# Kernel optimization log

Measured on AMD Instinct MI355X. Metric: run time of the kernel, lower is better.

Reference implementation:

```python
import jax, jax.numpy as jnp
import numpy as np

DIM, HEADS, DHEAD, CTX_DIM, DFF = 1280, 20, 64, 768, 5120
EPS = 1e-5
SCALE = DHEAD ** -0.5


def layer_norm(x, g, b):
    mu = jnp.mean(x, axis=-1, keepdims=True)
    var = jnp.mean(jnp.square(x - mu), axis=-1, keepdims=True)
    return (x - mu) * jax.lax.rsqrt(var + EPS) * g + b


def cross_attention(x, ctx, wq, wk, wv, wo, bo):
    B, N, _ = x.shape
    M = ctx.shape[1]
    q = jnp.einsum('bne,ef->bnf', x, wq).reshape(B, N, HEADS, DHEAD).transpose(0, 2, 1, 3)
    k = jnp.einsum('bme,ef->bmf', ctx, wk).reshape(B, M, HEADS, DHEAD).transpose(0, 2, 1, 3)
    v = jnp.einsum('bme,ef->bmf', ctx, wv).reshape(B, M, HEADS, DHEAD).transpose(0, 2, 1, 3)
    scores = jnp.einsum('bhnd,bhmd->bhnm', q, k) * SCALE
    attn = jax.nn.softmax(scores, axis=-1)
    out = jnp.einsum('bhnm,bhmd->bhnd', attn, v)
    out = out.transpose(0, 2, 1, 3).reshape(B, N, HEADS * DHEAD)
    return jnp.einsum('bnf,fe->bne', out, wo) + bo


def geglu_ff(x, w1, b1, w2, b2):
    h = jnp.einsum('bne,ef->bnf', x, w1) + b1  # [B,N,2*DFF]
    a, gate = h[..., :DFF], h[..., DFF:]
    h = a * jax.nn.gelu(gate)
    return jnp.einsum('bnf,fe->bne', h, w2) + b2


def block_forward(x, context,
                  g1, be1, wq1, wk1, wv1, wo1, bo1,
                  g2, be2, wq2, wk2, wv2, wo2, bo2,
                  g3, be3, w_ff1, b_ff1, w_ff2, b_ff2):
    x = cross_attention(layer_norm(x, g1, be1), layer_norm(x, g1, be1), wq1, wk1, wv1, wo1, bo1) + x
    x = cross_attention(layer_norm(x, g2, be2), context, wq2, wk2, wv2, wo2, bo2) + x
    return geglu_ff(layer_norm(x, g3, be3), w_ff1, b_ff1, w_ff2, b_ff2) + x


def setup_inputs() -> dict:
    key = jax.random.key(0)
    ks = jax.random.split(key, 20)
    s = 0.02
    inner = HEADS * DHEAD
    return {
        'x': jax.random.normal(ks[0], (4, 1024, DIM), jnp.float32),
        'context': jax.random.normal(ks[1], (4, 77, CTX_DIM), jnp.float32),
        'g1': jnp.ones((DIM,), jnp.float32), 'be1': jnp.zeros((DIM,), jnp.float32),
        'wq1': jax.random.normal(ks[2], (DIM, inner), jnp.float32) * s,
        'wk1': jax.random.normal(ks[3], (DIM, inner), jnp.float32) * s,
        'wv1': jax.random.normal(ks[4], (DIM, inner), jnp.float32) * s,
        'wo1': jax.random.normal(ks[5], (inner, DIM), jnp.float32) * s,
        'bo1': jnp.zeros((DIM,), jnp.float32),
        'g2': jnp.ones((DIM,), jnp.float32), 'be2': jnp.zeros((DIM,), jnp.float32),
        'wq2': jax.random.normal(ks[6], (DIM, inner), jnp.float32) * s,
        'wk2': jax.random.normal(ks[7], (CTX_DIM, inner), jnp.float32) * s,
        'wv2': jax.random.normal(ks[8], (CTX_DIM, inner), jnp.float32) * s,
        'wo2': jax.random.normal(ks[9], (inner, DIM), jnp.float32) * s,
        'bo2': jnp.zeros((DIM,), jnp.float32),
        'g3': jnp.ones((DIM,), jnp.float32), 'be3': jnp.zeros((DIM,), jnp.float32),
        'w_ff1': jax.random.normal(ks[10], (DIM, 2 * DFF), jnp.float32) * s,
        'b_ff1': jnp.zeros((2 * DFF,), jnp.float32),
        'w_ff2': jax.random.normal(ks[11], (DFF, DIM), jnp.float32) * s,
        'b_ff2': jnp.zeros((DIM,), jnp.float32),
    }


def reference(x, context,
              g1, be1, wq1, wk1, wv1, wo1, bo1,
              g2, be2, wq2, wk2, wv2, wo2, bo2,
              g3, be3, w_ff1, b_ff1, w_ff2, b_ff2):
    return block_forward(x, context,
                         g1, be1, wq1, wk1, wv1, wo1, bo1,
                         g2, be2, wq2, wk2, wv2, wo2, bo2,
                         g3, be3, w_ff1, b_ff1, w_ff2, b_ff2)
```

## Files before the change

### kernel.cpp

```cpp
#include <hip/hip_runtime.h>

typedef unsigned short u16;
typedef __bf16 bf16x8 __attribute__((ext_vector_type(8)));
typedef float f32x4 __attribute__((ext_vector_type(4)));

static __device__ __forceinline__ float bf2f(u16 u) {
    union { unsigned int i; float f; } v; v.i = ((unsigned int)u) << 16; return v.f;
}
static __device__ __forceinline__ u16 f2bf(float f) {
    union { float f; unsigned int i; } v; v.f = f;
    unsigned int b = v.i;
    b += 0x7fffu + ((b >> 16) & 1u);
    return (u16)(b >> 16);
}
static __device__ __forceinline__ u16 ldbf(const void* p, size_t i, int isf32) {
    return isf32 ? f2bf(((const float*)p)[i]) : ((const u16*)p)[i];
}
static __device__ __forceinline__ float ldf(const void* p, size_t i, int isf32) {
    return isf32 ? ((const float*)p)[i] : bf2f(((const u16*)p)[i]);
}
static __device__ __forceinline__ void glds16(const u16* g, u16* l) {
    __builtin_amdgcn_global_load_lds(
        (const __attribute__((address_space(1))) unsigned int*)g,
        (__attribute__((address_space(3))) unsigned int*)l,
        16, 0, 0);
}
static __device__ __forceinline__ int xcd_swz(int lid, int nwg) {
    return ((nwg & 7) == 0) ? ((lid & 7) * (nwg >> 3) + (lid >> 3)) : lid;
}

__global__ __launch_bounds__(256) void k_detect(const u16* __restrict__ xu, int* __restrict__ flag) {
    u16 v = xu[threadIdx.x * 2];
    int e = (v >> 7) & 0xFF;
    int sane = (e >= 87 && e <= 133) ? 1 : 0;
    int total = __syncthreads_count(sane);
    if (threadIdx.x == 0) flag[0] = (total < 192) ? 1 : 0;
}

__global__ __launch_bounds__(256) void k_b2f(const void* __restrict__ in, float* __restrict__ out, int n,
                                             const int* __restrict__ flagp) {
    int isf32 = *flagp;
    int i = blockIdx.x * 256 + threadIdx.x;
    if (i < n) out[i] = ldf(in, i, isf32);
}

__global__ __launch_bounds__(256) void k_cvt(const void* __restrict__ in, u16* __restrict__ out, int n,
                                             const int* __restrict__ flagp) {
    int isf32 = *flagp;
    int i = blockIdx.x * 256 + threadIdx.x;
    if (i < n) out[i] = ldbf(in, i, isf32);
}

__global__ __launch_bounds__(256) void k_addp(float* __restrict__ X, const float* __restrict__ P, int n4) {
    int i = blockIdx.x * 256 + threadIdx.x;
    int stride = gridDim.x * 256;
    for (; i < n4; i += stride) {
        f32x4 a = ((const f32x4*)X)[i];
        f32x4 b = ((const f32x4*)P)[i];
        a[0] += b[0]; a[1] += b[1]; a[2] += b[2]; a[3] += b[3];
        ((f32x4*)X)[i] = a;
    }
}

__global__ __launch_bounds__(256) void k_transpose(const void* __restrict__ W, u16* __restrict__ Wt,
                                                   int K, int N, const int* __restrict__ flagp) {
    int isf32 = *flagp;
    __shared__ u16 T[32][33];
    int k0 = blockIdx.x * 32, n0 = blockIdx.y * 32;
    int tid = threadIdx.x;
    int c = tid & 31, rr = tid >> 5;
    #pragma unroll
    for (int j = 0; j < 4; ++j) {
        int k = rr + j * 8;
        T[k][c] = ldbf(W, (size_t)(k0 + k) * N + n0 + c, isf32);
    }
    __syncthreads();
    #pragma unroll
    for (int j = 0; j < 4; ++j) {
        int n = rr + j * 8;
        Wt[(size_t)(n0 + n) * K + k0 + c] = T[c][n];
    }
}

__global__ __launch_bounds__(256) void k_transpose3(const void* __restrict__ W0, const void* __restrict__ W1,
                                                    const void* __restrict__ W2,
                                                    u16* __restrict__ D0, u16* __restrict__ D1,
                                                    u16* __restrict__ D2,
                                                    int K, int N, const int* __restrict__ flagp) {
    int isf32 = *flagp;
    int z = blockIdx.z;
    const void* W = (z == 0) ? W0 : (z == 1) ? W1 : W2;
    u16* Wt = (z == 0) ? D0 : (z == 1) ? D1 : D2;
    __shared__ u16 T[32][33];
    int k0 = blockIdx.x * 32, n0 = blockIdx.y * 32;
    int tid = threadIdx.x;
    int c = tid & 31, rr = tid >> 5;
    #pragma unroll
    for (int j = 0; j < 4; ++j) {
        int k = rr + j * 8;
        T[k][c] = ldbf(W, (size_t)(k0 + k) * N + n0 + c, isf32);
    }
    __syncthreads();
    #pragma unroll
    for (int j = 0; j < 4; ++j) {
        int n = rr + j * 8;
        Wt[(size_t)(n0 + n) * K + k0 + c] = T[c][n];
    }
}

__global__ __launch_bounds__(256) void k_layernorm(float* __restrict__ X, const float* __restrict__ P,
                                                   const void* __restrict__ G, const void* __restrict__ Bb,
                                                   u16* __restrict__ Y, int D,
                                                   const int* __restrict__ flagp) {
    int isf32 = *flagp;
    int row = blockIdx.x;
    float* xr = X + (size_t)row * D;
    const float* pr = P ? (P + (size_t)row * D) : nullptr;
    float s = 0.f, s2 = 0.f;
    for (int i = threadIdx.x; i < D; i += 256) {
        float v = xr[i] + (P ? pr[i] : 0.f);
        s += v; s2 += v * v;
    }
    #pragma unroll
    for (int off = 32; off; off >>= 1) { s += __shfl_down(s, off); s2 += __shfl_down(s2, off); }
    __shared__ float rs[4], rs2[4];
    __shared__ float stat[2];
    int w = threadIdx.x >> 6;
    if ((threadIdx.x & 63) == 0) { rs[w] = s; rs2[w] = s2; }
    __syncthreads();
    if (threadIdx.x == 0) {
        float ts = rs[0] + rs[1] + rs[2] + rs[3];
        float ts2 = rs2[0] + rs2[1] + rs2[2] + rs2[3];
        float mu = ts / D;
        float var = ts2 / D - mu * mu;
        stat[0] = mu; stat[1] = rsqrtf(var + 1e-5f);
    }
    __syncthreads();
    float mu = stat[0], rstd = stat[1];
    u16* yr = Y + (size_t)row * D;
    for (int i = threadIdx.x; i < D; i += 256) {
        float v = xr[i] + (P ? pr[i] : 0.f);
        if (P) xr[i] = v;
        yr[i] = f2bf((v - mu) * rstd * ldf(G, i, isf32) + ldf(Bb, i, isf32));
    }
}

template <int EPI>
__global__ __launch_bounds__(512, 2) void k_gemm8(const u16* __restrict__ A, const u16* __restrict__ Bt,
                                                  void* __restrict__ Cout, const void* __restrict__ bias,
                                                  int M, int N, int K, const int* __restrict__ flagp) {
    __shared__ __align__(16) u16 sm[65536];
    const int tid = threadIdx.x;
    const int w = tid >> 6;
    const int lane = tid & 63;
    const int quad = lane >> 4, r = lane & 15;
    const int wm = w >> 2, wn = w & 3;
    const int lid = blockIdx.x + blockIdx.y * gridDim.x;
    const int nid = xcd_swz(lid, gridDim.x * gridDim.y);
    const int row0 = (nid % gridDim.x) * 256;
    const int col0 = (nid / gridDim.x) * 256;
    const int NT = K >> 6;

    const u16* aP[2][2];
    const u16* bP[2][2];
    #pragma unroll
    for (int j = 0; j < 2; ++j) {
        int c = tid + w * 64 + j * 64;
        int rj = c >> 3;
        int qe = (c & 7) ^ (rj & 7);
        #pragma unroll
        for (int h = 0; h < 2; ++h) {
            int gr = h * 128 + rj;
            aP[h][j] = A + (size_t)(row0 + gr) * K + qe * 8;
            int n = col0 + gr;
            int m = (EPI == 1) ? (((n >> 4) & 1) * 5120 + (n >> 5) * 16 + (n & 15)) : n;
            bP[h][j] = Bt + (size_t)m * K + qe * 8;
        }
    }
    auto stageA = [&](int h, int t) {
        u16* base = sm + (t & 1) * 32768 + h * 8192 + w * 1024;
        glds16(aP[h][0] + t * 64, base);
        glds16(aP[h][1] + t * 64, base + 512);
    };
    auto stageB = [&](int h, int t) {
        u16* base = sm + (t & 1) * 32768 + 16384 + h * 8192 + w * 1024;
        glds16(bP[h][0] + t * 64, base);
        glds16(bP[h][1] + t * 64, base + 512);
    };

    f32x4 acc[2][2][4][2] = {};
    const int xq = r & 7;
    bf16x8 afA[4][2], afB[4][2], bf0[2][2], bf1[2][2];

    auto readA = [&](bf16x8 (&dst)[4][2], int Ab, int half) {
        #pragma unroll
        for (int i = 0; i < 4; ++i) {
            int ar = half * 128 + wm * 64 + i * 16 + r;
            #pragma unroll
            for (int ks = 0; ks < 2; ++ks)
                dst[i][ks] = *(const bf16x8*)(sm + Ab + ar * 64 + (((ks * 4 + quad) ^ xq) * 8));
        }
    };
    auto readB = [&](bf16x8 (&dst)[2][2], int Bb, int half) {
        #pragma unroll
        for (int g = 0; g < 2; ++g) {
            int br = half * 128 + wn * 32 + g * 16 + r;
            #pragma unroll
            for (int ks = 0; ks < 2; ++ks)
                dst[g][ks] = *(const bf16x8*)(sm + Bb + br * 64 + (((ks * 4 + quad) ^ xq) * 8));
        }
    };
    auto domfma = [&](int qm, int qn, bf16x8 (&a)[4][2], bf16x8 (&b)[2][2]) {
        #pragma unroll
        for (int ks = 0; ks < 2; ++ks)
            #pragma unroll
            for (int i = 0; i < 4; ++i)
                #pragma unroll
                for (int g = 0; g < 2; ++g)
                    acc[qm][qn][i][g] = __builtin_amdgcn_mfma_f32_16x16x32_bf16(
                        a[i][ks], b[g][ks], acc[qm][qn][i][g], 0, 0, 0);
    };

    stageA(0, 0); stageB(0, 0); stageA(1, 0); stageB(1, 0);
    if (NT > 1) {
        stageA(0, 1); stageB(0, 1);
        asm volatile("s_waitcnt vmcnt(4)" ::: "memory");
    } else {
        asm volatile("s_waitcnt vmcnt(0)" ::: "memory");
    }
    __builtin_amdgcn_s_barrier();
    readA(afA, 0, 0);
    readB(bf0, 16384, 0);

    for (int t = 0; t < NT; ++t) {
        const int Ab = (t & 1) * 32768;
        const int Bb = Ab + 16384;
        const int Abn = ((t + 1) & 1) * 32768;
        readB(bf1, Bb, 1);
        __builtin_amdgcn_sched_barrier(0);
        __builtin_amdgcn_s_setprio(1);
        domfma(0, 0, afA, bf0);
        __builtin_amdgcn_s_setprio(0);
        if (t + 1 < NT) stageA(1, t + 1);
        __builtin_amdgcn_s_barrier();
        readA(afB, Ab, 1);
        __builtin_amdgcn_sched_barrier(0);
        __builtin_amdgcn_s_setprio(1);
        domfma(0, 1, afA, bf1);
        __builtin_amdgcn_s_setprio(0);
        if (t + 1 < NT) stageB(1, t + 1);
        __builtin_amdgcn_s_barrier();
        __builtin_amdgcn_s_setprio(1);
        domfma(1, 1, afB, bf1);
        __builtin_amdgcn_s_setprio(0);
        if (t + 2 < NT) stageA(0, t + 2);
        __builtin_amdgcn_s_barrier();
        __builtin_amdgcn_s_setprio(1);
        domfma(1, 0, afB, bf0);
        __builtin_amdgcn_s_setprio(0);
        if (t + 2 < NT) stageB(0, t + 2);
        if (t + 2 < NT) asm volatile("s_waitcnt vmcnt(4)" ::: "memory");
        else            asm volatile("s_waitcnt vmcnt(0)" ::: "memory");
        __builtin_amdgcn_s_barrier();
        if (t + 1 < NT) {
            readA(afA, Abn, 0);
            readB(bf0, Abn + 16384, 0);
        }
    }

    if (EPI == 0) {
        u16* C = (u16*)Cout;
        #pragma unroll
        for (int qm = 0; qm < 2; ++qm) {
            #pragma unroll
            for (int qn = 0; qn < 2; ++qn) {
                #pragma unroll
                for (int i = 0; i < 4; ++i) {
                    int grow = row0 + qm * 128 + wm * 64 + i * 16 + quad * 4;
                    #pragma unroll
                    for (int g = 0; g < 2; ++g) {
                        int gcol = col0 + qn * 128 + wn * 32 + g * 16 + r;
                        #pragma unroll
                        for (int t4 = 0; t4 < 4; ++t4)
                            C[(size_t)(grow + t4) * N + gcol] = f2bf(acc[qm][qn][i][g][t4]);
                    }
                }
            }
        }
    } else {
        const int isf32 = *flagp;
        u16* C = (u16*)Cout;
        #pragma unroll
        for (int qm = 0; qm < 2; ++qm) {
            #pragma unroll
            for (int qn = 0; qn < 2; ++qn) {
                int ncb = col0 + qn * 128 + wn * 32;
                int oc = (ncb >> 1) + r;
                float bva = ldf(bias, oc, isf32);
                float bvu = ldf(bias, 5120 + oc, isf32);
                #pragma unroll
                for (int i = 0; i < 4; ++i) {
                    int grow = row0 + qm * 128 + wm * 64 + i * 16 + quad * 4;
                    #pragma unroll
                    for (int t4 = 0; t4 < 4; ++t4) {
                        float a = acc[qm][qn][i][0][t4] + bva;
                        float u = acc[qm][qn][i][1][t4] + bvu;
                        float z2 = 1.5957691216f * (u + 0.044715f * u * u * u);
                        float gl = u * __builtin_amdgcn_rcpf(1.f + __expf(-z2));
                        C[(size_t)(grow + t4) * 5120 + oc] = f2bf(a * gl);
                    }
                }
            }
        }
    }
}

template <int EPI>
__global__ __launch_bounds__(256) void k_gemm_t(const u16* __restrict__ A, const u16* __restrict__ Bt,
                                                void* __restrict__ Cout, float* __restrict__ Rf,
                                                const void* __restrict__ bias,
                                                int M, int N, int K, const int* __restrict__ flagp) {
    int isf32 = *flagp;
    __shared__ __align__(16) u16 As[4096];
    __shared__ __align__(16) u16 Bs[4096];
    int tid = threadIdx.x;
    int row0 = blockIdx.x * 128, col0 = blockIdx.y * 128;
    int S = gridDim.z, kz = blockIdx.z;
    int kseg = K / S;
    int kb = kz * kseg, ke = kb + kseg;
    int wave = tid >> 6, lane = tid & 63;
    int wm = (wave >> 1) * 64, wn = (wave & 1) * 64;
    int quad = lane >> 4, r = lane & 15;
    int c0 = wave * 64 + lane, c1 = 256 + c0;
    int ar0 = c0 >> 2, aq0 = (c0 & 3) ^ ((ar0 >> 1) & 3);
    int ar1 = c1 >> 2, aq1 = (c1 & 3) ^ ((ar1 >> 1) & 3);
    const u16* Ag0 = A + (size_t)min(row0 + ar0, M - 1) * K + aq0 * 8;
    const u16* Ag1 = A + (size_t)min(row0 + ar1, M - 1) * K + aq1 * 8;
    const u16* Bg0 = Bt + (size_t)(col0 + ar0) * K + aq0 * 8;
    const u16* Bg1 = Bt + (size_t)(col0 + ar1) * K + aq1 * 8;
    u16* lA0 = As + wave * 512;
    u16* lA1 = As + 2048 + wave * 512;
    u16* lB0 = Bs + wave * 512;
    u16* lB1 = Bs + 2048 + wave * 512;
    f32x4 acc[4][4] = {};
    for (int k0 = kb; k0 < ke; k0 += 32) {
        __syncthreads();
        glds16(Ag0 + k0, lA0);
        glds16(Ag1 + k0, lA1);
        glds16(Bg0 + k0, lB0);
        glds16(Bg1 + k0, lB1);
        __syncthreads();
        bf16x8 af[4], bfv[4];
        #pragma unroll
        for (int i = 0; i < 4; ++i) {
            int row = wm + i * 16 + r;
            af[i] = *(const bf16x8*)(As + (row * 4 + (quad ^ ((row >> 1) & 3))) * 8);
        }
        #pragma unroll
        for (int g = 0; g < 4; ++g) {
            int row = wn + g * 16 + r;
            bfv[g] = *(const bf16x8*)(Bs + (row * 4 + (quad ^ ((row >> 1) & 3))) * 8);
        }
        #pragma unroll
        for (int i = 0; i < 4; ++i)
            #pragma unroll
            for (int g = 0; g < 4; ++g)
                acc[i][g] = __builtin_amdgcn_mfma_f32_16x16x32_bf16(af[i], bfv[g], acc[i][g], 0, 0, 0);
    }
    #pragma unroll
    for (int i = 0; i < 4; ++i) {
        int grow = row0 + wm + i * 16 + quad * 4;
        if (grow >= M) continue;
        #pragma unroll
        for (int g = 0; g < 4; ++g) {
            int gcol = col0 + wn + g * 16 + r;
            float bv = (EPI == 2 && kz == 0) ? ldf(bias, gcol, isf32) : 0.f;
            #pragma unroll
            for (int t = 0; t < 4; ++t) {
                float v = acc[i][g][t];
                size_t off = (size_t)(grow + t) * N + gcol;
                if (EPI == 0) {
                    ((u16*)Cout)[off] = f2bf(v);
                } else {
                    if (kz == 0) Rf[off] += v + bv;
                    else         ((float*)Cout)[off] = v;
                }
            }
        }
    }
}

__global__ __launch_bounds__(256) void k_geglu_t(const u16* __restrict__ A, const u16* __restrict__ Bt,
                                                 const void* __restrict__ bias, u16* __restrict__ Out,
                                                 int M, int K, const int* __restrict__ flagp) {
    const int Nout = 5120;
    int isf32 = *flagp;
    __shared__ __align__(16) u16 As[4096];
    __shared__ __align__(16) u16 Bs[4096];
    int tid = threadIdx.x;
    int row0 = blockIdx.x * 128, col0 = blockIdx.y * 64;
    int wave = tid >> 6, lane = tid & 63;
    int quad = lane >> 4, r = lane & 15;
    int c0 = wave * 64 + lane, c1 = 256 + c0;
    int ar0 = c0 >> 2, aq0 = (c0 & 3) ^ ((ar0 >> 1) & 3);
    int ar1 = c1 >> 2, aq1 = (c1 & 3) ^ ((ar1 >> 1) & 3);
    const u16* Ag0 = A + (size_t)min(row0 + ar0, M - 1) * K + aq0 * 8;
    const u16* Ag1 = A + (size_t)min(row0 + ar1, M - 1) * K + aq1 * 8;
    const u16* Bg0 = Bt + (size_t)((ar0 >> 6) * Nout + col0 + (ar0 & 63)) * K + aq0 * 8;
    const u16* Bg1 = Bt + (size_t)((ar1 >> 6) * Nout + col0 + (ar1 & 63)) * K + aq1 * 8;
    u16* lA0 = As + wave * 512;
    u16* lA1 = As + 2048 + wave * 512;
    u16* lB0 = Bs + wave * 512;
    u16* lB1 = Bs + 2048 + wave * 512;
    f32x4 acc[2][2][4] = {};
    for (int k0 = 0; k0 < K; k0 += 32) {
        __syncthreads();
        glds16(Ag0 + k0, lA0);
        glds16(Ag1 + k0, lA1);
        glds16(Bg0 + k0, lB0);
        glds16(Bg1 + k0, lB1);
        __syncthreads();
        bf16x8 af[2], bv[2][4];
        #pragma unroll
        for (int i = 0; i < 2; ++i) {
            int row = wave * 32 + i * 16 + r;
            af[i] = *(const bf16x8*)(As + (row * 4 + (quad ^ ((row >> 1) & 3))) * 8);
        }
        #pragma unroll
        for (int p = 0; p < 2; ++p)
            #pragma unroll
            for (int g = 0; g < 4; ++g) {
                int row = p * 64 + g * 16 + r;
                bv[p][g] = *(const bf16x8*)(Bs + (row * 4 + (quad ^ ((row >> 1) & 3))) * 8);
            }
        #pragma unroll
        for (int p = 0; p < 2; ++p)
            #pragma unroll
            for (int i = 0; i < 2; ++i)
                #pragma unroll
                for (int g = 0; g < 4; ++g)
                    acc[p][i][g] = __builtin_amdgcn_mfma_f32_16x16x32_bf16(af[i], bv[p][g], acc[p][i][g], 0, 0, 0);
    }
    #pragma unroll
    for (int i = 0; i < 2; ++i) {
        int grow = row0 + wave * 32 + i * 16 + quad * 4;
        #pragma unroll
        for (int g = 0; g < 4; ++g) {
            int gcol = col0 + g * 16 + r;
            float bva = ldf(bias, gcol, isf32);
            float bvu = ldf(bias, Nout + gcol, isf32);
            #pragma unroll
            for (int t = 0; t < 4; ++t) {
                float a = acc[0][i][g][t] + bva;
                float u = acc[1][i][g][t] + bvu;
                float z2 = 1.5957691216f * (u + 0.044715f * u * u * u);
                float gl = u * __builtin_amdgcn_rcpf(1.f + __expf(-z2));
                Out[(size_t)(grow + t) * Nout + gcol] = f2bf(a * gl);
            }
        }
    }
}

template <int EPI, bool AEXT>
__global__ __launch_bounds__(256) void k_gemm(const void* __restrict__ A, const void* __restrict__ B,
                                              void* __restrict__ Cout, float* __restrict__ Rf,
                                              const void* __restrict__ bias,
                                              int M, int N, int K, const int* __restrict__ flagp) {
    int isf32 = *flagp;
    __shared__ u16 As[64][40];
    __shared__ u16 Bs[64][40];
    int tid = threadIdx.x;
    int row0 = blockIdx.x * 64, col0 = blockIdx.y * 64;
    int wave = tid >> 6, lane = tid & 63;
    int wm = (wave >> 1) * 32, wn = (wave & 1) * 32;
    int quad = lane >> 4, r = lane & 15;
    int arow = tid >> 2, akk = (tid & 3) * 8;
    int bnl = tid & 63, bkk = (tid >> 6) * 8;
    int garow = row0 + arow;
    f32x4 acc[2][2] = {};
    for (int k0 = 0; k0 < K; k0 += 32) {
        uint4 aval = {0u, 0u, 0u, 0u};
        if (garow < M) {
            if (AEXT && isf32) {
                const float* Af = (const float*)A;
                u16 t[8];
                #pragma unroll
                for (int j = 0; j < 8; ++j) t[j] = f2bf(Af[(size_t)garow * K + k0 + akk + j]);
                aval = *(uint4*)t;
            } else {
                aval = *(const uint4*)((const u16*)A + (size_t)garow * K + k0 + akk);
            }
        }
        u16 btmp[8];
        #pragma unroll
        for (int j = 0; j < 8; ++j) btmp[j] = ldbf(B, (size_t)(k0 + bkk + j) * N + col0 + bnl, isf32);
        __syncthreads();
        *(uint4*)(&As[arow][akk]) = aval;
        *(uint4*)(&Bs[bnl][bkk]) = *(uint4*)btmp;
        __syncthreads();
        bf16x8 a0 = *(const bf16x8*)(&As[wm + r][quad * 8]);
        bf16x8 a1 = *(const bf16x8*)(&As[wm + 16 + r][quad * 8]);
        bf16x8 b0 = *(const bf16x8*)(&Bs[wn + r][quad * 8]);
        bf16x8 b1 = *(const bf16x8*)(&Bs[wn + 16 + r][quad * 8]);
        acc[0][0] = __builtin_amdgcn_mfma_f32_16x16x32_bf16(a0, b0, acc[0][0], 0, 0, 0);
        acc[0][1] = __builtin_amdgcn_mfma_f32_16x16x32_bf16(a0, b1, acc[0][1], 0, 0, 0);
        acc[1][0] = __builtin_amdgcn_mfma_f32_16x16x32_bf16(a1, b0, acc[1][0], 0, 0, 0);
        acc[1][1] = __builtin_amdgcn_mfma_f32_16x16x32_bf16(a1, b1, acc[1][1], 0, 0, 0);
    }
    #pragma unroll
    for (int i = 0; i < 2; ++i)
        #pragma unroll
        for (int jn = 0; jn < 2; ++jn)
            #pragma unroll
            for (int t = 0; t < 4; ++t) {
                int grow = row0 + wm + i * 16 + quad * 4 + t;
                int gcol = col0 + wn + jn * 16 + r;
                if (grow >= M) continue;
                float v = acc[i][jn][t];
                size_t off = (size_t)grow * N + gcol;
                if (EPI == 0) {
                    ((u16*)Cout)[off] = f2bf(v);
                } else if (EPI == 2) {
                    Rf[off] += v + ldf(bias, gcol, isf32);
                } else {
                    ((float*)Cout)[off] = v + ldf(bias, gcol, isf32) + Rf[off];
                }
            }
}

__global__ __launch_bounds__(256) void k_gemm_geglu(const u16* __restrict__ A, const void* __restrict__ B,
                                                    const void* __restrict__ bias, u16* __restrict__ Out,
                                                    int M, int Nout, int K, int ldb,
                                                    const int* __restrict__ flagp) {
    int isf32 = *flagp;
    __shared__ u16 As[64][40];
    __shared__ u16 Bs[64][40];
    int tid = threadIdx.x;
    int row0 = blockIdx.x * 64, col0 = blockIdx.y * 64;
    int wave = tid >> 6, lane = tid & 63;
    int wm = (wave >> 1) * 32, wn = (wave & 1) * 32;
    int quad = lane >> 4, r = lane & 15;
    int arow = tid >> 2, akk = (tid & 3) * 8;
    int bnl = tid & 63, bkk = (tid >> 6) * 8;
    int garow = row0 + arow;
    f32x4 acc[2][2][2] = {};
    for (int p = 0; p < 2; ++p) {
        for (int k0 = 0; k0 < K; k0 += 32) {
            uint4 aval = {0u, 0u, 0u, 0u};
            if (garow < M) aval = *(const uint4*)(A + (size_t)garow * K + k0 + akk);
            u16 btmp[8];
            #pragma unroll
            for (int j = 0; j < 8; ++j)
                btmp[j] = ldbf(B, (size_t)(k0 + bkk + j) * ldb + p * Nout + col0 + bnl, isf32);
            __syncthreads();
            *(uint4*)(&As[arow][akk]) = aval;
            *(uint4*)(&Bs[bnl][bkk]) = *(uint4*)btmp;
            __syncthreads();
            bf16x8 a0 = *(const bf16x8*)(&As[wm + r][quad * 8]);
            bf16x8 a1 = *(const bf16x8*)(&As[wm + 16 + r][quad * 8]);
            bf16x8 b0 = *(const bf16x8*)(&Bs[wn + r][quad * 8]);
            bf16x8 b1 = *(const bf16x8*)(&Bs[wn + 16 + r][quad * 8]);
            acc[p][0][0] = __builtin_amdgcn_mfma_f32_16x16x32_bf16(a0, b0, acc[p][0][0], 0, 0, 0);
            acc[p][0][1] = __builtin_amdgcn_mfma_f32_16x16x32_bf16(a0, b1, acc[p][0][1], 0, 0, 0);
            acc[p][1][0] = __builtin_amdgcn_mfma_f32_16x16x32_bf16(a1, b0, acc[p][1][0], 0, 0, 0);
            acc[p][1][1] = __builtin_amdgcn_mfma_f32_16x16x32_bf16(a1, b1, acc[p][1][1], 0, 0, 0);
        }
    }
    #pragma unroll
    for (int i = 0; i < 2; ++i)
        #pragma unroll
        for (int jn = 0; jn < 2; ++jn)
            #pragma unroll
            for (int t = 0; t < 4; ++t) {
                int grow = row0 + wm + i * 16 + quad * 4 + t;
                int gcol = col0 + wn + jn * 16 + r;
                if (grow >= M) continue;
                float a = acc[0][i][jn][t] + ldf(bias, gcol, isf32);
                float u = acc[1][i][jn][t] + ldf(bias, Nout + gcol, isf32);
                float th = tanhf(0.7978845608f * (u + 0.044715f * u * u * u));
                float gl = 0.5f * u * (1.f + th);
                Out[(size_t)grow * Nout + gcol] = f2bf(a * gl);
            }
}

__global__ __launch_bounds__(256) void k_attn_flash(const u16* __restrict__ Q, const u16* __restrict__ K,
                                                    const u16* __restrict__ V, u16* __restrict__ O,
                                                    int N, int Mkv, int H, int ldq, int ldkv, int ldo) {
    __shared__ u16 Sp[4][16][40];
    __shared__ u16 VT[64][40];
    int nt = N / 64;
    int qt = blockIdx.x % nt;
    int bh = blockIdx.x / nt;
    int h = bh % H, b = bh / H;
    int tid = threadIdx.x, wave = tid >> 6, lane = tid & 63;
    int quad = lane >> 4, r = lane & 15;
    int q0 = qt * 64 + wave * 16;

    const u16* qbase = Q + ((size_t)(b * N + q0 + r)) * ldq + h * 64;
    bf16x8 aq0 = *(const bf16x8*)(qbase + quad * 8);
    bf16x8 aq1 = *(const bf16x8*)(qbase + 32 + quad * 8);

    f32x4 accO[4] = {};
    float m_i[4] = {-1e30f, -1e30f, -1e30f, -1e30f};
    float l_i[4] = {0.f, 0.f, 0.f, 0.f};

    int vkv = tid & 31, vdg = tid >> 5;

    for (int kv0 = 0; kv0 < Mkv; kv0 += 32) {
        int kr0 = min(kv0 + r, Mkv - 1);
        int kr1 = min(kv0 + 16 + r, Mkv - 1);
        const u16* kb0 = K + ((size_t)(b * Mkv + kr0)) * ldkv + h * 64;
        const u16* kb1 = K + ((size_t)(b * Mkv + kr1)) * ldkv + h * 64;
        bf16x8 bk00 = *(const bf16x8*)(kb0 + quad * 8);
        bf16x8 bk01 = *(const bf16x8*)(kb0 + 32 + quad * 8);
        bf16x8 bk10 = *(const bf16x8*)(kb1 + quad * 8);
        bf16x8 bk11 = *(const bf16x8*)(kb1 + 32 + quad * 8);
        int vrow = min(kv0 + vkv, Mkv - 1);
        uint4 vv = *(const uint4*)(V + ((size_t)(b * Mkv + vrow)) * ldkv + h * 64 + vdg * 8);

        __syncthreads();
        VT[vdg * 8 + 0][vkv] = (u16)(vv.x);
        VT[vdg * 8 + 1][vkv] = (u16)(vv.x >> 16);
        VT[vdg * 8 + 2][vkv] = (u16)(vv.y);
        VT[vdg * 8 + 3][vkv] = (u16)(vv.y >> 16);
        VT[vdg * 8 + 4][vkv] = (u16)(vv.z);
        VT[vdg * 8 + 5][vkv] = (u16)(vv.z >> 16);
        VT[vdg * 8 + 6][vkv] = (u16)(vv.w);
        VT[vdg * 8 + 7][vkv] = (u16)(vv.w >> 16);
        __syncthreads();

        f32x4 s0 = {}, s1 = {};
        s0 = __builtin_amdgcn_mfma_f32_16x16x32_bf16(aq0, bk00, s0, 0, 0, 0);
        s0 = __builtin_amdgcn_mfma_f32_16x16x32_bf16(aq1, bk01, s0, 0, 0, 0);
        s1 = __builtin_amdgcn_mfma_f32_16x16x32_bf16(aq0, bk10, s1, 0, 0, 0);
        s1 = __builtin_amdgcn_mfma_f32_16x16x32_bf16(aq1, bk11, s1, 0, 0, 0);
        bool mask0 = (kv0 + r) >= Mkv;
        bool mask1 = (kv0 + 16 + r) >= Mkv;

        #pragma unroll
        for (int t = 0; t < 4; ++t) {
            float a = mask0 ? -1e30f : s0[t] * 0.125f;
            float c = mask1 ? -1e30f : s1[t] * 0.125f;
            float mx = fmaxf(a, c);
            mx = fmaxf(mx, __shfl_xor(mx, 1));
            mx = fmaxf(mx, __shfl_xor(mx, 2));
            mx = fmaxf(mx, __shfl_xor(mx, 4));
            mx = fmaxf(mx, __shfl_xor(mx, 8));
            float mn = fmaxf(m_i[t], mx);
            float alpha = __expf(m_i[t] - mn);
            float p0 = __expf(a - mn);
            float p1 = __expf(c - mn);
            float ps = p0 + p1;
            ps += __shfl_xor(ps, 1);
            ps += __shfl_xor(ps, 2);
            ps += __shfl_xor(ps, 4);
            ps += __shfl_xor(ps, 8);
            l_i[t] = l_i[t] * alpha + ps;
            m_i[t] = mn;
            accO[0][t] *= alpha; accO[1][t] *= alpha; accO[2][t] *= alpha; accO[3][t] *= alpha;
            Sp[wave][quad * 4 + t][r] = f2bf(p0);
            Sp[wave][quad * 4 + t][16 + r] = f2bf(p1);
        }

        bf16x8 ap = *(const bf16x8*)(&Sp[wave][r][quad * 8]);
        #pragma unroll
        for (int g = 0; g < 4; ++g) {
            bf16x8 bvv = *(const bf16x8*)(&VT[g * 16 + r][quad * 8]);
            accO[g] = __builtin_amdgcn_mfma_f32_16x16x32_bf16(ap, bvv, accO[g], 0, 0, 0);
        }
    }

    u16* ob = O + ((size_t)(b * N + q0)) * ldo + h * 64;
    #pragma unroll
    for (int t = 0; t < 4; ++t) {
        float inv = 1.f / l_i[t];
        #pragma unroll
        for (int g = 0; g < 4; ++g)
            ob[(size_t)(quad * 4 + t) * ldo + g * 16 + r] = f2bf(accO[g][t] * inv);
    }
}

extern "C" void kernel_launch(void* const* d_in, const int* in_sizes, int n_in,
                              void* d_out, int out_size, void* d_ws, size_t ws_size,
                              hipStream_t stream) {
    const void* x    = d_in[0];
    const void* ctx  = d_in[1];
    const void* g1   = d_in[2];
    const void* be1  = d_in[3];
    const void* wq1  = d_in[4];
    const void* wk1  = d_in[5];
    const void* wv1  = d_in[6];
    const void* wo1  = d_in[7];
    const void* bo1  = d_in[8];
    const void* g2   = d_in[9];
    const void* be2  = d_in[10];
    const void* wq2  = d_in[11];
    const void* wk2  = d_in[12];
    const void* wv2  = d_in[13];
    const void* wo2  = d_in[14];
    const void* bo2  = d_in[15];
    const void* g3   = d_in[16];
    const void* be3  = d_in[17];
    const void* wff1 = d_in[18];
    const void* bff1 = d_in[19];
    const void* wff2 = d_in[20];
    const void* bff2 = d_in[21];

    const int BT = 4096, D = 1280;
    dim3 blk(256);
    char* ws = (char*)d_ws;

    const size_t NEED_FAST = 117393664;
    if (ws_size >= NEED_FAST) {
        int*   flag   = (int*)(ws);
        u16* lnout    = (u16*)(ws + 256);
        u16* qkv      = (u16*)(ws + 10486016);
        u16* attnout  = (u16*)(ws + 10486016 + 31457280);
        u16* gbuf     = (u16*)(ws + 10486016);
        u16* ctxb     = (u16*)(ws + 52429056);
        u16* kv2      = (u16*)(ws + 52902144);
        u16* wqkv1t   = (u16*)(ws + 54479104);
        u16* wo1t     = (u16*)(ws + 64309504);
        u16* wq2t     = (u16*)(ws + 67586304);
        u16* wkv2t    = (u16*)(ws + 70863104);
        u16* wo2t     = (u16*)(ws + 74795264);
        u16* wff1t    = (u16*)(ws + 78072064);
        u16* wff2t    = (u16*)(ws + 104286464);
        float* pff2   = (float*)(ws + 54479104);
        float* pWO    = (float*)(ws + 10486016);
        float* xres   = (float*)d_out;

        k_detect<<<dim3(1), blk, 0, stream>>>((const u16*)x, flag);
        k_b2f<<<dim3((BT * D + 255) / 256), blk, 0, stream>>>(x, xres, BT * D, flag);
        k_transpose3<<<dim3(40, 40, 3), blk, 0, stream>>>(wq1, wk1, wv1,
                                                          wqkv1t, wqkv1t + 1280 * 1280,
                                                          wqkv1t + 2 * 1280 * 1280, 1280, 1280, flag);
        k_transpose3<<<dim3(40, 40, 3), blk, 0, stream>>>(wo1, wq2, wo2,
                                                          wo1t, wq2t, wo2t, 1280, 1280, flag);
        k_transpose3<<<dim3(24, 40, 2), blk, 0, stream>>>(wk2, wv2, wv2,
                                                          wkv2t, wkv2t + 1280 * 768,
                                                          wkv2t + 1280 * 768, 768, 1280, flag);
        k_transpose<<<dim3(40, 320), blk, 0, stream>>>(wff1, wff1t, 1280, 10240, flag);
        k_transpose<<<dim3(160, 40), blk, 0, stream>>>(wff2, wff2t, 5120, 1280, flag);
        k_cvt<<<dim3((308 * 768 + 255) / 256), blk, 0, stream>>>(ctx, ctxb, 308 * 768, flag);
        k_layernorm<<<dim3(BT), blk, 0, stream>>>(xres, nullptr, g1, be1, lnout, D, flag);
        k_gemm8<0><<<dim3(16, 15), dim3(512), 0, stream>>>(lnout, wqkv1t, qkv, nullptr, BT, 3840, D, flag);
        k_attn_flash<<<dim3(16 * 80), blk, 0, stream>>>(qkv, qkv + 1280, qkv + 2560, attnout,
                                                        1024, 1024, 20, 3840, 3840, 1280);
        k_gemm_t<2><<<dim3(32, 10, 2), blk, 0, stream>>>(attnout, wo1t, pWO, xres, bo1, BT, D, D, flag);
        k_layernorm<<<dim3(BT), blk, 0, stream>>>(xres, pWO, g2, be2, lnout, D, flag);
        k_gemm_t<0><<<dim3(32, 10), blk, 0, stream>>>(lnout, wq2t, qkv, nullptr, nullptr, BT, D, D, flag);
        k_gemm_t<0><<<dim3(3, 20), blk, 0, stream>>>(ctxb, wkv2t, kv2, nullptr, nullptr, 308, 2560, 768, flag);
        k_attn_flash<<<dim3(16 * 80), blk, 0, stream>>>(qkv, kv2, kv2 + 1280, attnout,
                                                        1024, 77, 20, 1280, 2560, 1280);
        k_gemm_t<2><<<dim3(32, 10, 2), blk, 0, stream>>>(attnout, wo2t, pWO, xres, bo2, BT, D, D, flag);
        k_layernorm<<<dim3(BT), blk, 0, stream>>>(xres, pWO, g3, be3, lnout, D, flag);
        k_gemm8<1><<<dim3(16, 40), dim3(512), 0, stream>>>(lnout, wff1t, gbuf, bff1, BT, 10240, D, flag);
        k_gemm_t<2><<<dim3(32, 10, 2), blk, 0, stream>>>(gbuf, wff2t, pff2, xres, bff2, BT, D, 5120, flag);
        k_addp<<<dim3(2048), blk, 0, stream>>>(xres, pff2, BT * D / 4);
    } else {
        int*   flag    = (int*)(ws);
        float* xres    = (float*)(ws + 256);
        u16* lnout     = (u16*)(ws + 20971776);
        u16* q         = (u16*)(ws + 31457536);
        u16* kbuf      = (u16*)(ws + 41943296);
        u16* vbuf      = (u16*)(ws + 52429056);
        u16* attnout   = (u16*)(ws + 62914816);
        u16* k2        = (u16*)(ws + 73400576);
        u16* v2        = (u16*)(ws + 74189056);
        u16* gbuf      = (u16*)(ws + 31457536);

        dim3 g_gemm(64, 20);
        dim3 g_kv(5, 20);
        dim3 g_attn(16 * 80);

        k_detect<<<dim3(1), blk, 0, stream>>>((const u16*)x, flag);
        k_b2f<<<dim3((BT * D + 255) / 256), blk, 0, stream>>>(x, xres, BT * D, flag);
        k_layernorm<<<dim3(BT), blk, 0, stream>>>(xres, nullptr, g1, be1, lnout, D, flag);
        k_gemm<0, false><<<g_gemm, blk, 0, stream>>>(lnout, wq1, q, nullptr, nullptr, BT, D, D, flag);
        k_gemm<0, false><<<g_gemm, blk, 0, stream>>>(lnout, wk1, kbuf, nullptr, nullptr, BT, D, D, flag);
        k_gemm<0, false><<<g_gemm, blk, 0, stream>>>(lnout, wv1, vbuf, nullptr, nullptr, BT, D, D, flag);
        k_attn_flash<<<g_attn, blk, 0, stream>>>(q, kbuf, vbuf, attnout, 1024, 1024, 20, 1280, 1280, 1280);
        k_gemm<2, false><<<g_gemm, blk, 0, stream>>>(attnout, wo1, nullptr, xres, bo1, BT, D, D, flag);
        k_layernorm<<<dim3(BT), blk, 0, stream>>>(xres, nullptr, g2, be2, lnout, D, flag);
        k_gemm<0, false><<<g_gemm, blk, 0, stream>>>(lnout, wq2, q, nullptr, nullptr, BT, D, D, flag);
        k_gemm<0, true><<<g_kv, blk, 0, stream>>>(ctx, wk2, k2, nullptr, nullptr, 308, D, 768, flag);
        k_gemm<0, true><<<g_kv, blk, 0, stream>>>(ctx, wv2, v2, nullptr, nullptr, 308, D, 768, flag);
        k_attn_flash<<<g_attn, blk, 0, stream>>>(q, k2, v2, attnout, 1024, 77, 20, 1280, 1280, 1280);
        k_gemm<2, false><<<g_gemm, blk, 0, stream>>>(attnout, wo2, nullptr, xres, bo2, BT, D, D, flag);
        k_layernorm<<<dim3(BT), blk, 0, stream>>>(xres, nullptr, g3, be3, lnout, D, flag);
        k_gemm_geglu<<<dim3(64, 80), blk, 0, stream>>>(lnout, wff1, bff1, gbuf, BT, 5120, D, 10240, flag);
        k_gemm<3, false><<<g_gemm, blk, 0, stream>>>(gbuf, wff2, d_out, xres, bff2, BT, D, 5120, flag);
    }
}
```

Before: 831.4 us.

## Widen flash attention kv tile to 64 with K staged in LDS and exp2 softmax

The flash attention loop now processes 64 keys per iteration instead of 32. K and V tiles are loaded cooperatively into shared memory and shared by all four waves, rather than each wave loading K directly from global memory. Softmax folds log2(e) into the scale and uses exp2f. This cuts loop iterations, barriers and redundant K traffic, at the cost of more LDS and registers and more masked work for the short 77-token context.

```diff
diff --git a/kernel.cpp b/kernel.cpp
--- a/kernel.cpp
+++ b/kernel.cpp
@@ -586,8 +586,10 @@
 __global__ __launch_bounds__(256) void k_attn_flash(const u16* __restrict__ Q, const u16* __restrict__ K,
                                                     const u16* __restrict__ V, u16* __restrict__ O,
                                                     int N, int Mkv, int H, int ldq, int ldkv, int ldo) {
-    __shared__ u16 Sp[4][16][40];
-    __shared__ u16 VT[64][40];
+    __shared__ u16 KT[64][72];
+    __shared__ u16 VT[64][72];
+    __shared__ u16 Sp[4][16][72];
+    const float SC = 0.18033688f;
     int nt = N / 64;
     int qt = blockIdx.x % nt;
     int bh = blockIdx.x / nt;
@@ -604,53 +606,64 @@
     float m_i[4] = {-1e30f, -1e30f, -1e30f, -1e30f};
     float l_i[4] = {0.f, 0.f, 0.f, 0.f};
 
-    int vkv = tid & 31, vdg = tid >> 5;
-
-    for (int kv0 = 0; kv0 < Mkv; kv0 += 32) {
-        int kr0 = min(kv0 + r, Mkv - 1);
-        int kr1 = min(kv0 + 16 + r, Mkv - 1);
-        const u16* kb0 = K + ((size_t)(b * Mkv + kr0)) * ldkv + h * 64;
-        const u16* kb1 = K + ((size_t)(b * Mkv + kr1)) * ldkv + h * 64;
-        bf16x8 bk00 = *(const bf16x8*)(kb0 + quad * 8);
-        bf16x8 bk01 = *(const bf16x8*)(kb0 + 32 + quad * 8);
-        bf16x8 bk10 = *(const bf16x8*)(kb1 + quad * 8);
-        bf16x8 bk11 = *(const bf16x8*)(kb1 + 32 + quad * 8);
-        int vrow = min(kv0 + vkv, Mkv - 1);
-        uint4 vv = *(const uint4*)(V + ((size_t)(b * Mkv + vrow)) * ldkv + h * 64 + vdg * 8);
+    int srow = tid >> 2;
+    int scol = (tid & 3) * 8;
+
+    for (int kv0 = 0; kv0 < Mkv; kv0 += 64) {
+        int krow = min(kv0 + srow, Mkv - 1);
+        const u16* kp = K + ((size_t)(b * Mkv + krow)) * ldkv + h * 64;
+        const u16* vp = V + ((size_t)(b * Mkv + krow)) * ldkv + h * 64;
+        uint4 ka = *(const uint4*)(kp + scol);
+        uint4 kb = *(const uint4*)(kp + scol + 32);
+        uint4 va = *(const uint4*)(vp + scol);
+        uint4 vb = *(const uint4*)(vp + scol + 32);
 
         __syncthreads();
-        VT[vdg * 8 + 0][vkv] = (u16)(vv.x);
-        VT[vdg * 8 + 1][vkv] = (u16)(vv.x >> 16);
-        VT[vdg * 8 + 2][vkv] = (u16)(vv.y);
-        VT[vdg * 8 + 3][vkv] = (u16)(vv.y >> 16);
-        VT[vdg * 8 + 4][vkv] = (u16)(vv.z);
-        VT[vdg * 8 + 5][vkv] = (u16)(vv.z >> 16);
-        VT[vdg * 8 + 6][vkv] = (u16)(vv.w);
-        VT[vdg * 8 + 7][vkv] = (u16)(vv.w >> 16);
+        *(uint4*)(&KT[srow][scol]) = ka;
+        *(uint4*)(&KT[srow][scol + 32]) = kb;
+        u16 tmp[16];
+        *(uint4*)tmp = va; *(uint4*)(tmp + 8) = vb;
+        #pragma unroll
+        for (int j = 0; j < 8; ++j) {
+            VT[scol + j][srow] = tmp[j];
+            VT[scol + 32 + j][srow] = tmp[8 + j];
+        }
         __syncthreads();
 
-        f32x4 s0 = {}, s1 = {};
-        s0 = __builtin_amdgcn_mfma_f32_16x16x32_bf16(aq0, bk00, s0, 0, 0, 0);
-        s0 = __builtin_amdgcn_mfma_f32_16x16x32_bf16(aq1, bk01, s0, 0, 0, 0);
-        s1 = __builtin_amdgcn_mfma_f32_16x16x32_bf16(aq0, bk10, s1, 0, 0, 0);
-        s1 = __builtin_amdgcn_mfma_f32_16x16x32_bf16(aq1, bk11, s1, 0, 0, 0);
-        bool mask0 = (kv0 + r) >= Mkv;
-        bool mask1 = (kv0 + 16 + r) >= Mkv;
+        bf16x8 bk[4][2];
+        #pragma unroll
+        for (int g = 0; g < 4; ++g) {
+            bk[g][0] = *(const bf16x8*)(&KT[g * 16 + r][quad * 8]);
+            bk[g][1] = *(const bf16x8*)(&KT[g * 16 + r][32 + quad * 8]);
+        }
+        f32x4 s[4] = {};
+        #pragma unroll
+        for (int g = 0; g < 4; ++g) {
+            s[g] = __builtin_amdgcn_mfma_f32_16x16x32_bf16(aq0, bk[g][0], s[g], 0, 0, 0);
+            s[g] = __builtin_amdgcn_mfma_f32_16x16x32_bf16(aq1, bk[g][1], s[g], 0, 0, 0);
+        }
+        bool msk[4];
+        #pragma unroll
+        for (int g = 0; g < 4; ++g) msk[g] = (kv0 + g * 16 + r) >= Mkv;
 
         #pragma unroll
         for (int t = 0; t < 4; ++t) {
-            float a = mask0 ? -1e30f : s0[t] * 0.125f;
-            float c = mask1 ? -1e30f : s1[t] * 0.125f;
-            float mx = fmaxf(a, c);
+            float v0 = msk[0] ? -1e30f : s[0][t] * SC;
+            float v1 = msk[1] ? -1e30f : s[1][t] * SC;
+            float v2 = msk[2] ? -1e30f : s[2][t] * SC;
+            float v3 = msk[3] ? -1e30f : s[3][t] * SC;
+            float mx = fmaxf(fmaxf(v0, v1), fmaxf(v2, v3));
             mx = fmaxf(mx, __shfl_xor(mx, 1));
             mx = fmaxf(mx, __shfl_xor(mx, 2));
             mx = fmaxf(mx, __shfl_xor(mx, 4));
             mx = fmaxf(mx, __shfl_xor(mx, 8));
             float mn = fmaxf(m_i[t], mx);
-            float alpha = __expf(m_i[t] - mn);
-            float p0 = __expf(a - mn);
-            float p1 = __expf(c - mn);
-            float ps = p0 + p1;
+            float alpha = exp2f(m_i[t] - mn);
+            float p0 = exp2f(v0 - mn);
+            float p1 = exp2f(v1 - mn);
+            float p2 = exp2f(v2 - mn);
+            float p3 = exp2f(v3 - mn);
+            float ps = (p0 + p1) + (p2 + p3);
             ps += __shfl_xor(ps, 1);
             ps += __shfl_xor(ps, 2);
             ps += __shfl_xor(ps, 4);
@@ -658,15 +671,21 @@
             l_i[t] = l_i[t] * alpha + ps;
             m_i[t] = mn;
             accO[0][t] *= alpha; accO[1][t] *= alpha; accO[2][t] *= alpha; accO[3][t] *= alpha;
-            Sp[wave][quad * 4 + t][r] = f2bf(p0);
-            Sp[wave][quad * 4 + t][16 + r] = f2bf(p1);
-        }
-
-        bf16x8 ap = *(const bf16x8*)(&Sp[wave][r][quad * 8]);
+            int qr = quad * 4 + t;
+            Sp[wave][qr][r] = f2bf(p0);
+            Sp[wave][qr][16 + r] = f2bf(p1);
+            Sp[wave][qr][32 + r] = f2bf(p2);
+            Sp[wave][qr][48 + r] = f2bf(p3);
+        }
+
+        bf16x8 ap0 = *(const bf16x8*)(&Sp[wave][r][quad * 8]);
+        bf16x8 ap1 = *(const bf16x8*)(&Sp[wave][r][32 + quad * 8]);
         #pragma unroll
         for (int g = 0; g < 4; ++g) {
-            bf16x8 bvv = *(const bf16x8*)(&VT[g * 16 + r][quad * 8]);
-            accO[g] = __builtin_amdgcn_mfma_f32_16x16x32_bf16(ap, bvv, accO[g], 0, 0, 0);
+            bf16x8 bv0 = *(const bf16x8*)(&VT[g * 16 + r][quad * 8]);
+            bf16x8 bv1 = *(const bf16x8*)(&VT[g * 16 + r][32 + quad * 8]);
+            accO[g] = __builtin_amdgcn_mfma_f32_16x16x32_bf16(ap0, bv0, accO[g], 0, 0, 0);
+            accO[g] = __builtin_amdgcn_mfma_f32_16x16x32_bf16(ap1, bv1, accO[g], 0, 0, 0);
         }
     }
 
```

New measurement: 831.1 us. Within noise of the previous version (-0.0%).
